# Performance work log

Hardware: AMD Instinct MI355X
Metric: run time of the kernel (lower is better)

The kernel has to match this reference:

```python
import jax, jax.numpy as jnp
import numpy as np

N_NODES = 50000
N_EDGES = 1250000
D_IN = 64
D_HID = 64
D_OUT = 16
N_GRAPHS = 128


def setup_inputs() -> dict:
    key = jax.random.key(0)
    ks = jax.random.split(key, 16)
    glorot = lambda k, shape: jax.random.normal(k, shape, jnp.float32) * (2.0 / (shape[0] + shape[1])) ** 0.5
    inp = {
        "x": jax.random.normal(ks[0], (N_NODES, D_IN), jnp.float32),
        "edge_index": jax.random.randint(ks[1], (2, N_EDGES), 0, N_NODES, jnp.int32),
        "adj": jnp.zeros((1,), jnp.float32),
        "batch": jnp.sort(jax.random.randint(ks[2], (N_NODES,), 0, N_GRAPHS, jnp.int32)),
        # GraphConv layer 1: lin_rel (with bias) on aggregated msgs, lin_root (no bias) on x
        "W_rel1": glorot(ks[3], (D_IN, D_HID)),
        "b_rel1": jnp.zeros((D_HID,), jnp.float32),
        "W_root1": glorot(ks[4], (D_IN, D_HID)),
        "W_rel2": glorot(ks[5], (D_HID, D_HID)),
        "b_rel2": jnp.zeros((D_HID,), jnp.float32),
        "W_root2": glorot(ks[6], (D_HID, D_HID)),
        "W_rel3": glorot(ks[7], (D_HID, D_HID)),
        "b_rel3": jnp.zeros((D_HID,), jnp.float32),
        "W_root3": glorot(ks[8], (D_HID, D_HID)),
        "W_lin": glorot(ks[9], (D_HID, D_OUT)),
        "b_lin": jnp.zeros((D_OUT,), jnp.float32),
    }
    return inp


def graph_conv(x, src, dst, W_rel, b_rel, W_root):
    # PyG GraphConv (aggr='add'): out[i] = (sum_{j->i} x[j]) @ W_rel + b_rel + x[i] @ W_root
    agg = jax.ops.segment_sum(x[src], dst, num_segments=N_NODES)  # [N, d]
    return agg @ W_rel + b_rel + x @ W_root


def reference(x, edge_index, adj, batch,
              W_rel1, b_rel1, W_root1,
              W_rel2, b_rel2, W_root2,
              W_rel3, b_rel3, W_root3,
              W_lin, b_lin):
    src, dst = edge_index[0], edge_index[1]
    h = jax.nn.relu(graph_conv(x, src, dst, W_rel1, b_rel1, W_root1))
    h = jax.nn.relu(graph_conv(h, src, dst, W_rel2, b_rel2, W_root2))
    h = graph_conv(h, src, dst, W_rel3, b_rel3, W_root3)
    # global_mean_pool over batch ids
    sums = jax.ops.segment_sum(h, batch, num_segments=N_GRAPHS)  # [G, d]
    counts = jax.ops.segment_sum(jnp.ones((h.shape[0],), h.dtype), batch, num_segments=N_GRAPHS)
    pooled = sums / jnp.maximum(counts, 1.0)[:, None]
    return pooled @ W_lin + b_lin  # [G, D_OUT]
```

## Files before the change

kernel.cpp:

```cpp
#include <hip/hip_runtime.h>

#define D 64
#define N_GRAPHS 128
#define D_OUT 16
#define BCAP 16384
#define TILE 4096

typedef unsigned short u16;
typedef unsigned int u32;
typedef unsigned char u8;
typedef __attribute__((ext_vector_type(8))) short bf16x8;
typedef __attribute__((ext_vector_type(4))) float f32x4;
typedef __attribute__((ext_vector_type(2))) float f32x2;

__device__ inline u16 f2bf(float f) {
  u32 u = __float_as_uint(f);
  return (u16)((u + 0x7fffu + ((u >> 16) & 1u)) >> 16);
}
__device__ inline float bf2f(u16 b) { return __uint_as_float((u32)b << 16); }
__device__ inline f32x2 bfpair(u32 v) {
  return (f32x2){__uint_as_float(v << 16), __uint_as_float(v & 0xffff0000u)};
}

__global__ __launch_bounds__(256) void cvt_bf16_kernel(
    const float* __restrict__ in, u16* __restrict__ out, int n4,
    int* __restrict__ cursors, int nbuck,
    const float* __restrict__ Wrel1, const float* __restrict__ Wroot1,
    const float* __restrict__ Wrel2, const float* __restrict__ Wroot2,
    const float* __restrict__ Wrel3, const float* __restrict__ Wroot3,
    const float* __restrict__ Wlin, const float* __restrict__ brel3,
    const float* __restrict__ blin,
    float* __restrict__ M1, float* __restrict__ M2, float* __restrict__ cvec,
    u16* __restrict__ WbT1r, u16* __restrict__ WbT1o,
    u16* __restrict__ WbT2r, u16* __restrict__ WbT2o) {
  int t = threadIdx.x;
  if (blockIdx.x == 0) {
    if (t < nbuck) cursors[t] = t * BCAP;
    if (t >= 240) {
      int o = t - 240;
      float c = blin[o];
#pragma unroll
      for (int j = 0; j < D; j++) c = fmaf(brel3[j], Wlin[j * D_OUT + o], c);
      cvec[o] = c;
    }
  } else if (blockIdx.x <= 8) {
    int idx = (blockIdx.x - 1) * 256 + t;
    const float* W = (idx < 1024) ? Wrel3 : Wroot3;
    float* M = (idx < 1024) ? M1 : M2;
    int id = idx & 1023;
    int k = id >> 4, o = id & 15;
    float acc = 0.0f;
#pragma unroll
    for (int j = 0; j < D; j++) acc = fmaf(W[k * D + j], Wlin[j * D_OUT + o], acc);
    M[id] = acc;
  } else if (blockIdx.x <= 16) {
    int tid = (blockIdx.x - 9) * 256 + t;
    int mat = tid >> 9;
    int r = tid & 511;
    int o = r >> 3;
    int k0 = (r & 7) * 8;
    const float* Wsrc = (mat == 0) ? Wrel1 : (mat == 1) ? Wroot1
                       : (mat == 2) ? Wrel2 : Wroot2;
    u16* Wdst = (mat == 0) ? WbT1r : (mat == 1) ? WbT1o
               : (mat == 2) ? WbT2r : WbT2o;
    u16 tmp[8];
#pragma unroll
    for (int j = 0; j < 8; j++) tmp[j] = f2bf(Wsrc[(k0 + j) * D + o]);
    uint4 pw;
    pw.x = (u32)tmp[0] | ((u32)tmp[1] << 16);
    pw.y = (u32)tmp[2] | ((u32)tmp[3] << 16);
    pw.z = (u32)tmp[4] | ((u32)tmp[5] << 16);
    pw.w = (u32)tmp[6] | ((u32)tmp[7] << 16);
    *(uint4*)&Wdst[o * D + k0] = pw;
  }
  int i = blockIdx.x * 256 + t;
  if (i >= n4) return;
  float4 v = ((const float4*)in)[i];
  ushort4 o4;
  o4.x = f2bf(v.x); o4.y = f2bf(v.y); o4.z = f2bf(v.z); o4.w = f2bf(v.w);
  ((ushort4*)out)[i] = o4;
}

__global__ __launch_bounds__(256) void bin_kernel(
    const int* __restrict__ src, const int* __restrict__ dst,
    int* __restrict__ cursors, u32* __restrict__ binned,
    int n_edges, int nbuck) {
  __shared__ u32 ent[TILE];
  __shared__ u8 ebk[TILE];
  __shared__ int hist[256];
  __shared__ int startb[256];
  __shared__ int cur[256];
  __shared__ int gbase[256];
  int t = threadIdx.x;
  hist[t] = 0;
  __syncthreads();

  int base = blockIdx.x * TILE;
  int cnt = n_edges - base;
  if (cnt > TILE) cnt = TILE;

  int mys[16], myd[16];
#pragma unroll
  for (int j = 0; j < 16; j++) {
    int i = base + t + j * 256;
    if (t + j * 256 < cnt) {
      mys[j] = src[i];
      myd[j] = dst[i];
      atomicAdd(&hist[myd[j] >> 8], 1);
    } else {
      myd[j] = -1;
    }
  }
  __syncthreads();
  int myc = hist[t];
  for (int off = 1; off < 256; off <<= 1) {
    int tmp = (t >= off) ? hist[t - off] : 0;
    __syncthreads();
    hist[t] += tmp;
    __syncthreads();
  }
  int excl = hist[t] - myc;
  startb[t] = excl;
  cur[t] = excl;
  __syncthreads();

#pragma unroll
  for (int j = 0; j < 16; j++) {
    if (myd[j] >= 0) {
      int b = myd[j] >> 8;
      int p = atomicAdd(&cur[b], 1);
      ent[p] = ((u32)myd[j] << 16) | (u32)mys[j];
      ebk[p] = (u8)b;
    }
  }
  __syncthreads();

  if (t < nbuck && myc > 0) gbase[t] = atomicAdd(&cursors[t], myc);
  __syncthreads();

#pragma unroll
  for (int j = 0; j < 16; j++) {
    int p = t + j * 256;
    if (p < cnt) {
      int b = ebk[p];
      int gpos = gbase[b] + (p - startb[b]);
      if (gpos < (b + 1) * BCAP) binned[gpos] = ent[p];
    }
  }
}

__global__ __launch_bounds__(256) void csr_kernel(
    const u32* __restrict__ binned, const int* __restrict__ cursors,
    u16* __restrict__ csr_src, int* __restrict__ offsets,
    int n_nodes, int nbuck) {
  __shared__ int deg[256];
  __shared__ int cur[256];
  __shared__ int red[256];
  __shared__ u16 lcsr[BCAP];
  int b = blockIdx.x, t = threadIdx.x;
  int cnt = cursors[b] - b * BCAP;
  if (cnt < 0) cnt = 0;
  if (cnt > BCAP) cnt = BCAP;

  int c = 0;
  if (t < b) {
    c = cursors[t] - t * BCAP;
    if (c < 0) c = 0;
    if (c > BCAP) c = BCAP;
  }
  red[t] = c;
  __syncthreads();
  for (int off = 128; off > 0; off >>= 1) {
    if (t < off) red[t] += red[t + off];
    __syncthreads();
  }
  int ebase = red[0];

  int nodeBase = b << 8;
  int nn = n_nodes - nodeBase;
  if (nn > 256) nn = 256;

  deg[t] = 0;
  __syncthreads();
  const u32* be = binned + (size_t)b * BCAP;
  for (int i = t; i < cnt; i += 256)
    atomicAdd(&deg[(be[i] >> 16) - nodeBase], 1);
  __syncthreads();
  int myd = deg[t];
  for (int off = 1; off < 256; off <<= 1) {
    int tmp = (t >= off) ? deg[t - off] : 0;
    __syncthreads();
    deg[t] += tmp;
    __syncthreads();
  }
  int loff = deg[t] - myd;
  cur[t] = loff;
  if (t < nn) offsets[nodeBase + t] = ebase + loff;
  if (b == nbuck - 1 && t == 0) offsets[n_nodes] = ebase + cnt;
  __syncthreads();

  for (int i = t; i < cnt; i += 256) {
    u32 e = be[i];
    int ln = (e >> 16) - nodeBase;
    int p = atomicAdd(&cur[ln], 1);
    lcsr[p] = (u16)(e & 0xffffu);
  }
  __syncthreads();
  for (int i = t; i < cnt; i += 256) csr_src[ebase + i] = lcsr[i];
}

#define ACC8(a, r) \
  a[0] += bfpair(r.x); a[1] += bfpair(r.y); a[2] += bfpair(r.z); a[3] += bfpair(r.w);

#define BALANCE_PROLOGUE(soff, permAr, blockBase, n_nodes, offsets)     \
  {                                                                     \
    int t_ = threadIdx.x;                                               \
    if (t_ < 33) {                                                      \
      int idx = blockBase + t_;                                         \
      if (idx > n_nodes) idx = n_nodes;                                 \
      soff[t_] = offsets[idx];                                          \
    }                                                                   \
    __syncthreads();                                                    \
    if (t_ < 32) {                                                      \
      int d_ = (blockBase + t_ < n_nodes) ? soff[t_ + 1] - soff[t_] : -1; \
      int r_ = 0;                                                       \
      for (int j_ = 0; j_ < 32; j_++) {                                 \
        int dj_ = (blockBase + j_ < n_nodes) ? soff[j_ + 1] - soff[j_] : -1; \
        if (dj_ > d_ || (dj_ == d_ && j_ < t_)) r_++;                   \
      }                                                                 \
      permAr[r_] = (u8)t_;                                              \
    }                                                                   \
    __syncthreads();                                                    \
  }

__global__ __launch_bounds__(256) void fused_layer_kernel(
    const u16* __restrict__ h, const int* __restrict__ offsets,
    const u16* __restrict__ csr_src,
    const u16* __restrict__ WbTrel, const u16* __restrict__ WbTroot,
    const float* __restrict__ brel,
    u16* __restrict__ h_out, int n_nodes, int do_relu) {
  __shared__ __align__(16) u16 ldsA[32 * 72];
  __shared__ __align__(16) u16 ldsX[32 * 72];
  __shared__ int soff[33];
  __shared__ u8 permAr[32];
  int w = threadIdx.x >> 6;
  int lane = threadIdx.x & 63;
  int sub = lane >> 3;
  int fo = (lane & 7) * 8;
  int blockBase = blockIdx.x * 32;

  BALANCE_PROLOGUE(soff, permAr, blockBase, n_nodes, offsets)

  int ln = permAr[w * 8 + sub];
  int node = blockBase + ln;
  bool valid = node < n_nodes;
  int start = soff[ln];
  int end = soff[ln + 1];
  if (!valid) end = start;
  int lrow = ln * 72;

  uint4 xr = make_uint4(0, 0, 0, 0);
  if (valid) xr = *(const uint4*)(h + ((size_t)node << 6) + fo);
  *(uint4*)&ldsX[lrow + fo] = xr;

  f32x2 a0[4] = {{0,0},{0,0},{0,0},{0,0}};
  f32x2 a1[4] = {{0,0},{0,0},{0,0},{0,0}};
  int i = start;
  for (; i + 3 < end; i += 4) {
    int s0 = csr_src[i], s1 = csr_src[i + 1], s2 = csr_src[i + 2], s3 = csr_src[i + 3];
    uint4 r0 = *(const uint4*)(h + ((size_t)s0 << 6) + fo);
    uint4 r1 = *(const uint4*)(h + ((size_t)s1 << 6) + fo);
    uint4 r2 = *(const uint4*)(h + ((size_t)s2 << 6) + fo);
    uint4 r3 = *(const uint4*)(h + ((size_t)s3 << 6) + fo);
    ACC8(a0, r0) ACC8(a1, r1) ACC8(a0, r2) ACC8(a1, r3)
  }
  for (; i < end; i++) {
    int s0 = csr_src[i];
    uint4 r0 = *(const uint4*)(h + ((size_t)s0 << 6) + fo);
    ACC8(a0, r0)
  }
#pragma unroll
  for (int k = 0; k < 4; k++) a0[k] += a1[k];

  uint4 pa;
  pa.x = (u32)f2bf(a0[0].x) | ((u32)f2bf(a0[0].y) << 16);
  pa.y = (u32)f2bf(a0[1].x) | ((u32)f2bf(a0[1].y) << 16);
  pa.z = (u32)f2bf(a0[2].x) | ((u32)f2bf(a0[2].y) << 16);
  pa.w = (u32)f2bf(a0[3].x) | ((u32)f2bf(a0[3].y) << 16);
  *(uint4*)&ldsA[lrow + fo] = pa;
  __syncthreads();

  int mt = w & 1;
  int ntb = (w >> 1) * 2;
  int lr = lane & 15, lk = lane >> 4;
  int arow = (mt * 16 + lr) * 72;
  bf16x8 af0 = *(const bf16x8*)&ldsA[arow + lk * 8];
  bf16x8 af1 = *(const bf16x8*)&ldsA[arow + 32 + lk * 8];
  bf16x8 xf0 = *(const bf16x8*)&ldsX[arow + lk * 8];
  bf16x8 xf1 = *(const bf16x8*)&ldsX[arow + 32 + lk * 8];
#pragma unroll
  for (int tt = 0; tt < 2; tt++) {
    int nt = ntb + tt;
    int wrow = (nt * 16 + lr) * D + lk * 8;
    bf16x8 br0 = *(const bf16x8*)(WbTrel + wrow);
    bf16x8 br1 = *(const bf16x8*)(WbTrel + wrow + 32);
    bf16x8 bo0 = *(const bf16x8*)(WbTroot + wrow);
    bf16x8 bo1 = *(const bf16x8*)(WbTroot + wrow + 32);
    f32x4 acc = {0.0f, 0.0f, 0.0f, 0.0f};
    acc = __builtin_amdgcn_mfma_f32_16x16x32_bf16(af0, br0, acc, 0, 0, 0);
    acc = __builtin_amdgcn_mfma_f32_16x16x32_bf16(af1, br1, acc, 0, 0, 0);
    acc = __builtin_amdgcn_mfma_f32_16x16x32_bf16(xf0, bo0, acc, 0, 0, 0);
    acc = __builtin_amdgcn_mfma_f32_16x16x32_bf16(xf1, bo1, acc, 0, 0, 0);
    float bias = brel[nt * 16 + lr];
#pragma unroll
    for (int r = 0; r < 4; r++) {
      int onode = blockBase + mt * 16 + lk * 4 + r;
      if (onode < n_nodes) {
        float v = acc[r] + bias;
        if (do_relu) v = fmaxf(v, 0.0f);
        h_out[((size_t)onode << 6) + nt * 16 + lr] = f2bf(v);
      }
    }
  }
}

__global__ __launch_bounds__(256) void gather_kernel(
    const u16* __restrict__ h, const int* __restrict__ offsets,
    const u16* __restrict__ csr_src, float* __restrict__ agg, int n_nodes) {
  __shared__ int soff[33];
  __shared__ u8 permAr[32];
  int w = threadIdx.x >> 6;
  int lane = threadIdx.x & 63;
  int sub = lane >> 3;
  int fo = (lane & 7) * 8;
  int blockBase = blockIdx.x * 32;

  BALANCE_PROLOGUE(soff, permAr, blockBase, n_nodes, offsets)

  int ln = permAr[w * 8 + sub];
  int node = blockBase + ln;
  bool valid = node < n_nodes;
  int start = soff[ln];
  int end = soff[ln + 1];
  if (!valid) end = start;

  f32x2 a0[4] = {{0,0},{0,0},{0,0},{0,0}};
  f32x2 a1[4] = {{0,0},{0,0},{0,0},{0,0}};
  int i = start;
  for (; i + 3 < end; i += 4) {
    int s0 = csr_src[i], s1 = csr_src[i + 1], s2 = csr_src[i + 2], s3 = csr_src[i + 3];
    uint4 r0 = *(const uint4*)(h + ((size_t)s0 << 6) + fo);
    uint4 r1 = *(const uint4*)(h + ((size_t)s1 << 6) + fo);
    uint4 r2 = *(const uint4*)(h + ((size_t)s2 << 6) + fo);
    uint4 r3 = *(const uint4*)(h + ((size_t)s3 << 6) + fo);
    ACC8(a0, r0) ACC8(a1, r1) ACC8(a0, r2) ACC8(a1, r3)
  }
  for (; i < end; i++) {
    int s0 = csr_src[i];
    uint4 r0 = *(const uint4*)(h + ((size_t)s0 << 6) + fo);
    ACC8(a0, r0)
  }
#pragma unroll
  for (int k = 0; k < 4; k++) a0[k] += a1[k];
  if (valid) {
    float* ap = agg + ((size_t)node << 6) + fo;
    *(float4*)(ap)     = make_float4(a0[0].x, a0[0].y, a0[1].x, a0[1].y);
    *(float4*)(ap + 4) = make_float4(a0[2].x, a0[2].y, a0[3].x, a0[3].y);
  }
}

__global__ __launch_bounds__(256) void pool_final_kernel(
    const float* __restrict__ aggA, const u16* __restrict__ hH,
    const int* __restrict__ batch,
    const float* __restrict__ M1, const float* __restrict__ M2,
    const float* __restrict__ cvec, const float* __restrict__ blin,
    float* __restrict__ out, int n_nodes) {
  __shared__ int seg[2];
  __shared__ float redA[256], redH[256];
  __shared__ float mA[64], mH[64];
  int g = blockIdx.x;
  int t = threadIdx.x;
  if (t < 2) {
    int target = g + t;
    int lo = 0, hi = n_nodes;
    while (lo < hi) {
      int mid = (lo + hi) >> 1;
      if (batch[mid] < target) lo = mid + 1; else hi = mid;
    }
    seg[t] = lo;
  }
  __syncthreads();
  int start = seg[0], end = seg[1];
  int f = t & 63, sub = t >> 6;
  float aA = 0.0f, aH = 0.0f;
  for (int n = start + sub; n < end; n += 4) {
    aA += aggA[((size_t)n << 6) + f];
    aH += bf2f(hH[((size_t)n << 6) + f]);
  }
  redA[t] = aA;
  redH[t] = aH;
  __syncthreads();
  if (sub == 0) {
    float inv = (end > start) ? 1.0f / (float)(end - start) : 0.0f;
    mA[f] = (redA[f] + redA[64 + f] + redA[128 + f] + redA[192 + f]) * inv;
    mH[f] = (redH[f] + redH[64 + f] + redH[128 + f] + redH[192 + f]) * inv;
  }
  __syncthreads();
  if (t < 16) {
    float acc;
    if (end > start) {
      acc = cvec[t];
#pragma unroll
      for (int k = 0; k < D; k++)
        acc = fmaf(mA[k], M1[k * D_OUT + t], fmaf(mH[k], M2[k * D_OUT + t], acc));
    } else {
      acc = blin[t];
    }
    out[g * D_OUT + t] = acc;
  }
}

extern "C" void kernel_launch(void* const* d_in, const int* in_sizes, int n_in,
                              void* d_out, int out_size, void* d_ws, size_t ws_size,
                              hipStream_t stream) {
  const float* x     = (const float*)d_in[0];
  const int*   ei    = (const int*)d_in[1];
  const int*   batch = (const int*)d_in[3];
  const float* Wrel1 = (const float*)d_in[4];
  const float* brel1 = (const float*)d_in[5];
  const float* Wroot1= (const float*)d_in[6];
  const float* Wrel2 = (const float*)d_in[7];
  const float* brel2 = (const float*)d_in[8];
  const float* Wroot2= (const float*)d_in[9];
  const float* Wrel3 = (const float*)d_in[10];
  const float* brel3 = (const float*)d_in[11];
  const float* Wroot3= (const float*)d_in[12];
  const float* Wlin  = (const float*)d_in[13];
  const float* blin  = (const float*)d_in[14];
  float* out = (float*)d_out;

  const int n_edges = in_sizes[1] / 2;
  const int n_nodes = in_sizes[0] / D;
  const int* src = ei;
  const int* dst = ei + n_edges;
  const int nbuck = (n_nodes + 255) >> 8;

  char* p = (char*)d_ws;
  size_t binned_bytes = (size_t)nbuck * BCAP * sizeof(u32);
  size_t agg_bytes = (size_t)n_nodes * D * sizeof(float);
  u32* binned  = (u32*)p;
  float* agg   = (float*)p;
  p += (binned_bytes > agg_bytes ? binned_bytes : agg_bytes);
  float* M1     = (float*)p; p += (size_t)D * D_OUT * sizeof(float);
  float* M2     = (float*)p; p += (size_t)D * D_OUT * sizeof(float);
  float* cvec   = (float*)p; p += 16 * sizeof(float);
  int* cursors  = (int*)p;   p += 256 * sizeof(int);
  int* offsets  = (int*)p;   p += (size_t)(n_nodes + 4) * sizeof(int);
  u16* hX       = (u16*)p;   p += (size_t)n_nodes * D * sizeof(u16);
  u16* h1       = (u16*)p;   p += (size_t)n_nodes * D * sizeof(u16);
  u16* h2       = (u16*)p;   p += (size_t)n_nodes * D * sizeof(u16);
  u16* csr_src  = (u16*)p;   p += (size_t)n_edges * sizeof(u16);
  u16* WbT1r    = (u16*)p;   p += (size_t)D * D * sizeof(u16);
  u16* WbT1o    = (u16*)p;   p += (size_t)D * D * sizeof(u16);
  u16* WbT2r    = (u16*)p;   p += (size_t)D * D * sizeof(u16);
  u16* WbT2o    = (u16*)p;   p += (size_t)D * D * sizeof(u16);

  const int bin_blocks = (n_edges + TILE - 1) / TILE;
  const int fused_blocks = (n_nodes + 31) / 32;
  const int cvt_n4 = n_nodes * D / 4;

  cvt_bf16_kernel<<<(cvt_n4 + 255) / 256, 256, 0, stream>>>(
      x, hX, cvt_n4, cursors, nbuck, Wrel1, Wroot1, Wrel2, Wroot2,
      Wrel3, Wroot3, Wlin, brel3, blin, M1, M2, cvec,
      WbT1r, WbT1o, WbT2r, WbT2o);
  bin_kernel<<<bin_blocks, 256, 0, stream>>>(src, dst, cursors, binned, n_edges, nbuck);
  csr_kernel<<<nbuck, 256, 0, stream>>>(binned, cursors, csr_src, offsets, n_nodes, nbuck);

  fused_layer_kernel<<<fused_blocks, 256, 0, stream>>>(
      hX, offsets, csr_src, WbT1r, WbT1o, brel1, h1, n_nodes, 1);
  fused_layer_kernel<<<fused_blocks, 256, 0, stream>>>(
      h1, offsets, csr_src, WbT2r, WbT2o, brel2, h2, n_nodes, 1);

  gather_kernel<<<fused_blocks, 256, 0, stream>>>(h2, offsets, csr_src, agg, n_nodes);

  pool_final_kernel<<<N_GRAPHS, 256, 0, stream>>>(
      agg, h2, batch, M1, M2, cvec, blin, out, n_nodes);
}
```

Measured before the change: 257.7 us.

## Fuse conversion with binning, stage CSR indices in LDS, pool via atomics

Merges the bf16 conversion/weight-prep kernel with edge binning into one launch, with cursors zeroed by a memset instead of inside the kernel. Gather kernels now stage each block's CSR source indices in shared memory before the neighbour loop. The last gather accumulates per-graph sums directly with float atomics, which removes the full fp32 agg buffer and the pool pass that re-read it. The cost is heavy atomic contention on 128 graph rows, since batch is sorted and neighbouring nodes hit the same addresses, plus a nondeterministic summation order.

```diff
diff --git a/kernel.cpp b/kernel.cpp
--- a/kernel.cpp
+++ b/kernel.cpp
@@ -5,6 +5,7 @@
 #define D_OUT 16
 #define BCAP 16384
 #define TILE 4096
+#define ECAP 2048
 
 typedef unsigned short u16;
 typedef unsigned int u32;
@@ -22,9 +23,10 @@
   return (f32x2){__uint_as_float(v << 16), __uint_as_float(v & 0xffff0000u)};
 }
 
-__global__ __launch_bounds__(256) void cvt_bf16_kernel(
-    const float* __restrict__ in, u16* __restrict__ out, int n4,
-    int* __restrict__ cursors, int nbuck,
+__global__ __launch_bounds__(256) void cvtbin_kernel(
+    const float* __restrict__ xin, u16* __restrict__ hX, int n4, int nbin,
+    const int* __restrict__ src, const int* __restrict__ dst,
+    int* __restrict__ cursors, u32* __restrict__ binned, int n_edges, int nbuck,
     const float* __restrict__ Wrel1, const float* __restrict__ Wroot1,
     const float* __restrict__ Wrel2, const float* __restrict__ Wroot2,
     const float* __restrict__ Wrel3, const float* __restrict__ Wroot3,
@@ -33,9 +35,74 @@
     float* __restrict__ M1, float* __restrict__ M2, float* __restrict__ cvec,
     u16* __restrict__ WbT1r, u16* __restrict__ WbT1o,
     u16* __restrict__ WbT2r, u16* __restrict__ WbT2o) {
+  __shared__ u32 ent[TILE];
+  __shared__ u8 ebk[TILE];
+  __shared__ int hist[256];
+  __shared__ int startb[256];
+  __shared__ int cur[256];
+  __shared__ int gbase[256];
   int t = threadIdx.x;
-  if (blockIdx.x == 0) {
-    if (t < nbuck) cursors[t] = t * BCAP;
+
+  if ((int)blockIdx.x < nbin) {
+    hist[t] = 0;
+    __syncthreads();
+    int base = blockIdx.x * TILE;
+    int cnt = n_edges - base;
+    if (cnt > TILE) cnt = TILE;
+
+    int mys[16], myd[16];
+#pragma unroll
+    for (int j = 0; j < 16; j++) {
+      int i = base + t + j * 256;
+      if (t + j * 256 < cnt) {
+        mys[j] = src[i];
+        myd[j] = dst[i];
+        atomicAdd(&hist[myd[j] >> 8], 1);
+      } else {
+        myd[j] = -1;
+      }
+    }
+    __syncthreads();
+    int myc = hist[t];
+    for (int off = 1; off < 256; off <<= 1) {
+      int tmp = (t >= off) ? hist[t - off] : 0;
+      __syncthreads();
+      hist[t] += tmp;
+      __syncthreads();
+    }
+    int excl = hist[t] - myc;
+    startb[t] = excl;
+    cur[t] = excl;
+    __syncthreads();
+
+#pragma unroll
+    for (int j = 0; j < 16; j++) {
+      if (myd[j] >= 0) {
+        int b = myd[j] >> 8;
+        int p = atomicAdd(&cur[b], 1);
+        ent[p] = ((u32)myd[j] << 16) | (u32)mys[j];
+        ebk[p] = (u8)b;
+      }
+    }
+    __syncthreads();
+
+    if (t < nbuck && myc > 0) gbase[t] = atomicAdd(&cursors[t], myc);
+    __syncthreads();
+
+#pragma unroll
+    for (int j = 0; j < 16; j++) {
+      int p = t + j * 256;
+      if (p < cnt) {
+        int b = ebk[p];
+        int gpos = gbase[b] + (p - startb[b]);
+        if (gpos < BCAP) binned[(size_t)b * BCAP + gpos] = ent[p];
+      }
+    }
+    return;
+  }
+
+  int cb = blockIdx.x - nbin;
+  if (cb == 0) {
     if (t >= 240) {
       int o = t - 240;
       float c = blin[o];
@@ -43,8 +110,8 @@
       for (int j = 0; j < D; j++) c = fmaf(brel3[j], Wlin[j * D_OUT + o], c);
       cvec[o] = c;
     }
-  } else if (blockIdx.x <= 8) {
-    int idx = (blockIdx.x - 1) * 256 + t;
+  } else if (cb <= 8) {
+    int idx = (cb - 1) * 256 + t;
     const float* W = (idx < 1024) ? Wrel3 : Wroot3;
     float* M = (idx < 1024) ? M1 : M2;
     int id = idx & 1023;
@@ -53,8 +120,8 @@
 #pragma unroll
     for (int j = 0; j < D; j++) acc = fmaf(W[k * D + j], Wlin[j * D_OUT + o], acc);
     M[id] = acc;
-  } else if (blockIdx.x <= 16) {
-    int tid = (blockIdx.x - 9) * 256 + t;
+  } else if (cb <= 16) {
+    int tid = (cb - 9) * 256 + t;
     int mat = tid >> 9;
     int r = tid & 511;
     int o = r >> 3;
@@ -73,80 +140,12 @@
     pw.w = (u32)tmp[6] | ((u32)tmp[7] << 16);
     *(uint4*)&Wdst[o * D + k0] = pw;
   }
-  int i = blockIdx.x * 256 + t;
+  int i = cb * 256 + t;
   if (i >= n4) return;
-  float4 v = ((const float4*)in)[i];
+  float4 v = ((const float4*)xin)[i];
   ushort4 o4;
   o4.x = f2bf(v.x); o4.y = f2bf(v.y); o4.z = f2bf(v.z); o4.w = f2bf(v.w);
-  ((ushort4*)out)[i] = o4;
-}
-
-__global__ __launch_bounds__(256) void bin_kernel(
-    const int* __restrict__ src, const int* __restrict__ dst,
-    int* __restrict__ cursors, u32* __restrict__ binned,
-    int n_edges, int nbuck) {
-  __shared__ u32 ent[TILE];
-  __shared__ u8 ebk[TILE];
-  __shared__ int hist[256];
-  __shared__ int startb[256];
-  __shared__ int cur[256];
-  __shared__ int gbase[256];
-  int t = threadIdx.x;
-  hist[t] = 0;
-  __syncthreads();
-
-  int base = blockIdx.x * TILE;
-  int cnt = n_edges - base;
-  if (cnt > TILE) cnt = TILE;
-
-  int mys[16], myd[16];
-#pragma unroll
-  for (int j = 0; j < 16; j++) {
-    int i = base + t + j * 256;
-    if (t + j * 256 < cnt) {
-      mys[j] = src[i];
-      myd[j] = dst[i];
-      atomicAdd(&hist[myd[j] >> 8], 1);
-    } else {
-      myd[j] = -1;
-    }
-  }
-  __syncthreads();
-  int myc = hist[t];
-  for (int off = 1; off < 256; off <<= 1) {
-    int tmp = (t >= off) ? hist[t - off] : 0;
-    __syncthreads();
-    hist[t] += tmp;
-    __syncthreads();
-  }
-  int excl = hist[t] - myc;
-  startb[t] = excl;
-  cur[t] = excl;
-  __syncthreads();
-
-#pragma unroll
-  for (int j = 0; j < 16; j++) {
-    if (myd[j] >= 0) {
-      int b = myd[j] >> 8;
-      int p = atomicAdd(&cur[b], 1);
-      ent[p] = ((u32)myd[j] << 16) | (u32)mys[j];
-      ebk[p] = (u8)b;
-    }
-  }
-  __syncthreads();
-
-  if (t < nbuck && myc > 0) gbase[t] = atomicAdd(&cursors[t], myc);
-  __syncthreads();
-
-#pragma unroll
-  for (int j = 0; j < 16; j++) {
-    int p = t + j * 256;
-    if (p < cnt) {
-      int b = ebk[p];
-      int gpos = gbase[b] + (p - startb[b]);
-      if (gpos < (b + 1) * BCAP) binned[gpos] = ent[p];
-    }
-  }
+  ((ushort4*)hX)[i] = o4;
 }
 
 __global__ __launch_bounds__(256) void csr_kernel(
@@ -158,13 +157,13 @@
   __shared__ int red[256];
   __shared__ u16 lcsr[BCAP];
   int b = blockIdx.x, t = threadIdx.x;
-  int cnt = cursors[b] - b * BCAP;
+  int cnt = cursors[b];
   if (cnt < 0) cnt = 0;
   if (cnt > BCAP) cnt = BCAP;
 
   int c = 0;
   if (t < b) {
-    c = cursors[t] - t * BCAP;
+    c = cursors[t];
     if (c < 0) c = 0;
     if (c > BCAP) c = BCAP;
   }
@@ -212,7 +211,7 @@
 #define ACC8(a, r) \
   a[0] += bfpair(r.x); a[1] += bfpair(r.y); a[2] += bfpair(r.z); a[3] += bfpair(r.w);
 
-#define BALANCE_PROLOGUE(soff, permAr, blockBase, n_nodes, offsets)     \
+#define GATHER_PROLOGUE(soff, permAr, eidx, blockBase, n_nodes, offsets, csr_src, gsrc, ebase0, scnt) \
   {                                                                     \
     int t_ = threadIdx.x;                                               \
     if (t_ < 33) {                                                      \
@@ -221,6 +220,10 @@
       soff[t_] = offsets[idx];                                          \
     }                                                                   \
     __syncthreads();                                                    \
+    ebase0 = soff[0];                                                   \
+    int ecnt_ = soff[32] - ebase0;                                      \
+    scnt = ecnt_ < ECAP ? ecnt_ : ECAP;                                 \
+    gsrc = csr_src + ebase0;                                            \
     if (t_ < 32) {                                                      \
       int d_ = (blockBase + t_ < n_nodes) ? soff[t_ + 1] - soff[t_] : -1; \
       int r_ = 0;                                                       \
@@ -230,8 +233,11 @@
       }                                                                 \
       permAr[r_] = (u8)t_;                                              \
     }                                                                   \
+    for (int e_ = t_; e_ < scnt; e_ += 256) eidx[e_] = gsrc[e_];        \
     __syncthreads();                                                    \
   }
+
+#define IDX(i) ((i) < ECAP ? (int)eidx[i] : (int)gsrc[i])
 
 __global__ __launch_bounds__(256) void fused_layer_kernel(
     const u16* __restrict__ h, const int* __restrict__ offsets,
@@ -243,20 +249,23 @@
   __shared__ __align__(16) u16 ldsX[32 * 72];
   __shared__ int soff[33];
   __shared__ u8 permAr[32];
+  __shared__ u16 eidx[ECAP];
   int w = threadIdx.x >> 6;
   int lane = threadIdx.x & 63;
   int sub = lane >> 3;
   int fo = (lane & 7) * 8;
   int blockBase = blockIdx.x * 32;
-
-  BALANCE_PROLOGUE(soff, permAr, blockBase, n_nodes, offsets)
+  const u16* gsrc;
+  int ebase0, scnt;
+
+  GATHER_PROLOGUE(soff, permAr, eidx, blockBase, n_nodes, offsets, csr_src, gsrc, ebase0, scnt)
 
   int ln = permAr[w * 8 + sub];
   int node = blockBase + ln;
   bool valid = node < n_nodes;
-  int start = soff[ln];
-  int end = soff[ln + 1];
-  if (!valid) end = start;
+  int ls = soff[ln] - ebase0;
+  int le = soff[ln + 1] - ebase0;
+  if (!valid) le = ls;
   int lrow = ln * 72;
 
   uint4 xr = make_uint4(0, 0, 0, 0);
@@ -265,17 +274,17 @@
 
   f32x2 a0[4] = {{0,0},{0,0},{0,0},{0,0}};
   f32x2 a1[4] = {{0,0},{0,0},{0,0},{0,0}};
-  int i = start;
-  for (; i + 3 < end; i += 4) {
-    int s0 = csr_src[i], s1 = csr_src[i + 1], s2 = csr_src[i + 2], s3 = csr_src[i + 3];
+  int i = ls;
+  for (; i + 3 < le; i += 4) {
+    int s0 = IDX(i), s1 = IDX(i + 1), s2 = IDX(i + 2), s3 = IDX(i + 3);
     uint4 r0 = *(const uint4*)(h + ((size_t)s0 << 6) + fo);
     uint4 r1 = *(const uint4*)(h + ((size_t)s1 << 6) + fo);
     uint4 r2 = *(const uint4*)(h + ((size_t)s2 << 6) + fo);
     uint4 r3 = *(const uint4*)(h + ((size_t)s3 << 6) + fo);
     ACC8(a0, r0) ACC8(a1, r1) ACC8(a0, r2) ACC8(a1, r3)
   }
-  for (; i < end; i++) {
-    int s0 = csr_src[i];
+  for (; i < le; i++) {
+    int s0 = IDX(i);
     uint4 r0 = *(const uint4*)(h + ((size_t)s0 << 6) + fo);
     ACC8(a0, r0)
   }
@@ -324,60 +333,75 @@
   }
 }
 
-__global__ __launch_bounds__(256) void gather_kernel(
+__global__ __launch_bounds__(256) void gather_pool_kernel(
     const u16* __restrict__ h, const int* __restrict__ offsets,
-    const u16* __restrict__ csr_src, float* __restrict__ agg, int n_nodes) {
+    const u16* __restrict__ csr_src, const int* __restrict__ batch,
+    float* __restrict__ pooledA, float* __restrict__ pooledH, int n_nodes) {
   __shared__ int soff[33];
   __shared__ u8 permAr[32];
+  __shared__ u16 eidx[ECAP];
+  __shared__ int gid[32];
   int w = threadIdx.x >> 6;
   int lane = threadIdx.x & 63;
   int sub = lane >> 3;
   int fo = (lane & 7) * 8;
   int blockBase = blockIdx.x * 32;
-
-  BALANCE_PROLOGUE(soff, permAr, blockBase, n_nodes, offsets)
+  if (threadIdx.x < 32)
+    gid[threadIdx.x] = (blockBase + threadIdx.x < n_nodes) ? batch[blockBase + threadIdx.x] : 0;
+  const u16* gsrc;
+  int ebase0, scnt;
+
+  GATHER_PROLOGUE(soff, permAr, eidx, blockBase, n_nodes, offsets, csr_src, gsrc, ebase0, scnt)
 
   int ln = permAr[w * 8 + sub];
   int node = blockBase + ln;
   bool valid = node < n_nodes;
-  int start = soff[ln];
-  int end = soff[ln + 1];
-  if (!valid) end = start;
+  int ls = soff[ln] - ebase0;
+  int le = soff[ln + 1] - ebase0;
+  if (!valid) le = ls;
 
   f32x2 a0[4] = {{0,0},{0,0},{0,0},{0,0}};
   f32x2 a1[4] = {{0,0},{0,0},{0,0},{0,0}};
-  int i = start;
-  for (; i + 3 < end; i += 4) {
-    int s0 = csr_src[i], s1 = csr_src[i + 1], s2 = csr_src[i + 2], s3 = csr_src[i + 3];
+  int i = ls;
+  for (; i + 3 < le; i += 4) {
+    int s0 = IDX(i), s1 = IDX(i + 1), s2 = IDX(i + 2), s3 = IDX(i + 3);
     uint4 r0 = *(const uint4*)(h + ((size_t)s0 << 6) + fo);
     uint4 r1 = *(const uint4*)(h + ((size_t)s1 << 6) + fo);
     uint4 r2 = *(const uint4*)(h + ((size_t)s2 << 6) + fo);
     uint4 r3 = *(const uint4*)(h + ((size_t)s3 << 6) + fo);
     ACC8(a0, r0) ACC8(a1, r1) ACC8(a0, r2) ACC8(a1, r3)
   }
-  for (; i < end; i++) {
-    int s0 = csr_src[i];
+  for (; i < le; i++) {
+    int s0 = IDX(i);
     uint4 r0 = *(const uint4*)(h + ((size_t)s0 << 6) + fo);
     ACC8(a0, r0)
   }
 #pragma unroll
   for (int k = 0; k < 4; k++) a0[k] += a1[k];
+
   if (valid) {
-    float* ap = agg + ((size_t)node << 6) + fo;
-    *(float4*)(ap)     = make_float4(a0[0].x, a0[0].y, a0[1].x, a0[1].y);
-    *(float4*)(ap + 4) = make_float4(a0[2].x, a0[2].y, a0[3].x, a0[3].y);
-  }
-}
-
-__global__ __launch_bounds__(256) void pool_final_kernel(
-    const float* __restrict__ aggA, const u16* __restrict__ hH,
-    const int* __restrict__ batch,
+    int g = gid[ln];
+    uint4 xr = *(const uint4*)(h + ((size_t)node << 6) + fo);
+    f32x2 x0 = bfpair(xr.x), x1 = bfpair(xr.y), x2 = bfpair(xr.z), x3 = bfpair(xr.w);
+    float* pA = pooledA + g * D + fo;
+    float* pH = pooledH + g * D + fo;
+    atomicAdd(pA + 0, a0[0].x); atomicAdd(pA + 1, a0[0].y);
+    atomicAdd(pA + 2, a0[1].x); atomicAdd(pA + 3, a0[1].y);
+    atomicAdd(pA + 4, a0[2].x); atomicAdd(pA + 5, a0[2].y);
+    atomicAdd(pA + 6, a0[3].x); atomicAdd(pA + 7, a0[3].y);
+    atomicAdd(pH + 0, x0.x); atomicAdd(pH + 1, x0.y);
+    atomicAdd(pH + 2, x1.x); atomicAdd(pH + 3, x1.y);
+    atomicAdd(pH + 4, x2.x); atomicAdd(pH + 5, x2.y);
+    atomicAdd(pH + 6, x3.x); atomicAdd(pH + 7, x3.y);
+  }
+}
+
+__global__ __launch_bounds__(64) void final_kernel(
+    const float* __restrict__ pooledA, const float* __restrict__ pooledH,
     const float* __restrict__ M1, const float* __restrict__ M2,
     const float* __restrict__ cvec, const float* __restrict__ blin,
-    float* __restrict__ out, int n_nodes) {
+    const int* __restrict__ batch, float* __restrict__ out, int n_nodes) {
   __shared__ int seg[2];
-  __shared__ float redA[256], redH[256];
-  __shared__ float mA[64], mH[64];
   int g = blockIdx.x;
   int t = threadIdx.x;
   if (t < 2) {
@@ -390,33 +414,21 @@
     seg[t] = lo;
   }
   __syncthreads();
-  int start = seg[0], end = seg[1];
-  int f = t & 63, sub = t >> 6;
-  float aA = 0.0f, aH = 0.0f;
-  for (int n = start + sub; n < end; n += 4) {
-    aA += aggA[((size_t)n << 6) + f];
-    aH += bf2f(hH[((size_t)n << 6) + f]);
-  }
-  redA[t] = aA;
-  redH[t] = aH;
-  __syncthreads();
-  if (sub == 0) {
-    float inv = (end > start) ? 1.0f / (float)(end - start) : 0.0f;
-    mA[f] = (redA[f] + redA[64 + f] + redA[128 + f] + redA[192 + f]) * inv;
-    mH[f] = (redH[f] + redH[64 + f] + redH[128 + f] + redH[192 + f]) * inv;
-  }
-  __syncthreads();
-  if (t < 16) {
-    float acc;
-    if (end > start) {
-      acc = cvec[t];
+  int cnt = seg[1] - seg[0];
+  if (t < D_OUT) {
+    float res;
+    if (cnt > 0) {
+      float inv = 1.0f / (float)cnt;
+      float acc = cvec[t];
 #pragma unroll
       for (int k = 0; k < D; k++)
-        acc = fmaf(mA[k], M1[k * D_OUT + t], fmaf(mH[k], M2[k * D_OUT + t], acc));
+        acc = fmaf(pooledA[g * D + k] * inv, M1[k * D_OUT + t],
+              fmaf(pooledH[g * D + k] * inv, M2[k * D_OUT + t], acc));
+      res = acc;
     } else {
-      acc = blin[t];
-    }
-    out[g * D_OUT + t] = acc;
+      res = blin[t];
+    }
+    out[g * D_OUT + t] = res;
   }
 }
 
@@ -446,15 +458,13 @@
   const int nbuck = (n_nodes + 255) >> 8;
 
   char* p = (char*)d_ws;
-  size_t binned_bytes = (size_t)nbuck * BCAP * sizeof(u32);
-  size_t agg_bytes = (size_t)n_nodes * D * sizeof(float);
-  u32* binned  = (u32*)p;
-  float* agg   = (float*)p;
-  p += (binned_bytes > agg_bytes ? binned_bytes : agg_bytes);
+  u32* binned  = (u32*)p;    p += (size_t)nbuck * BCAP * sizeof(u32);
+  int* cursors = (int*)p;    p += 256 * sizeof(int);
+  float* pooledA = (float*)p; p += (size_t)N_GRAPHS * D * sizeof(float);
+  float* pooledH = (float*)p; p += (size_t)N_GRAPHS * D * sizeof(float);
   float* M1     = (float*)p; p += (size_t)D * D_OUT * sizeof(float);
   float* M2     = (float*)p; p += (size_t)D * D_OUT * sizeof(float);
   float* cvec   = (float*)p; p += 16 * sizeof(float);
-  int* cursors  = (int*)p;   p += 256 * sizeof(int);
   int* offsets  = (int*)p;   p += (size_t)(n_nodes + 4) * sizeof(int);
   u16* hX       = (u16*)p;   p += (size_t)n_nodes * D * sizeof(u16);
   u16* h1       = (u16*)p;   p += (size_t)n_nodes * D * sizeof(u16);
@@ -466,14 +476,17 @@
   u16* WbT2o    = (u16*)p;   p += (size_t)D * D * sizeof(u16);
 
   const int bin_blocks = (n_edges + TILE - 1) / TILE;
+  const int cvt_n4 = n_nodes * D / 4;
+  const int cvt_blocks = (cvt_n4 + 255) / 256;
   const int fused_blocks = (n_nodes + 31) / 32;
-  const int cvt_n4 = n_nodes * D / 4;
-
-  cvt_bf16_kernel<<<(cvt_n4 + 255) / 256, 256, 0, stream>>>(
-      x, hX, cvt_n4, cursors, nbuck, Wrel1, Wroot1, Wrel2, Wroot2,
-      Wrel3, Wroot3, Wlin, brel3, blin, M1, M2, cvec,
-      WbT1r, WbT1o, WbT2r, WbT2o);
-  bin_kernel<<<bin_blocks, 256, 0, stream>>>(src, dst, cursors, binned, n_edges, nbuck);
+
+  const size_t zero_bytes = 256 * sizeof(int) + 2 * (size_t)N_GRAPHS * D * sizeof(float);
+  hipMemsetAsync(cursors, 0, zero_bytes, stream);
+
+  cvtbin_kernel<<<bin_blocks + cvt_blocks, 256, 0, stream>>>(
+      x, hX, cvt_n4, bin_blocks, src, dst, cursors, binned, n_edges, nbuck,
+      Wrel1, Wroot1, Wrel2, Wroot2, Wrel3, Wroot3, Wlin, brel3, blin,
+      M1, M2, cvec, WbT1r, WbT1o, WbT2r, WbT2o);
   csr_kernel<<<nbuck, 256, 0, stream>>>(binned, cursors, csr_src, offsets, n_nodes, nbuck);
 
   fused_layer_kernel<<<fused_blocks, 256, 0, stream>>>(
@@ -481,8 +494,9 @@
   fused_layer_kernel<<<fused_blocks, 256, 0, stream>>>(
       h1, offsets, csr_src, WbT2r, WbT2o, brel2, h2, n_nodes, 1);
 
-  gather_kernel<<<fused_blocks, 256, 0, stream>>>(h2, offsets, csr_src, agg, n_nodes);
-
-  pool_final_kernel<<<N_GRAPHS, 256, 0, stream>>>(
-      agg, h2, batch, M1, M2, cvec, blin, out, n_nodes);
-}
+  gather_pool_kernel<<<fused_blocks, 256, 0, stream>>>(
+      h2, offsets, csr_src, batch, pooledA, pooledH, n_nodes);
+
+  final_kernel<<<N_GRAPHS, 64, 0, stream>>>(
+      pooledA, pooledH, M1, M2, cvec, blin, batch, out, n_nodes);
+}
```

After: 748.1 us. 2.9x slower.
